# Kernel tuning notes

Hardware: AMD Instinct MI355X
Metric: run time of the kernel (lower is better)

Reference implementation:

```python
import jax, jax.numpy as jnp
import numpy as np

D_MODEL = 1024
N_HEADS = 16
HEAD_DIM = D_MODEL // N_HEADS  # 64


def setup_inputs() -> dict:
    key = jax.random.key(0)
    ks = jax.random.split(key, 6)
    scale_in = 1.0 / np.sqrt(D_MODEL)
    scale_hd = 1.0 / np.sqrt(N_HEADS * HEAD_DIM)
    inputs_q = jax.random.normal(ks[0], (4, 2048, D_MODEL), dtype=jnp.float32)
    # DenseGeneral kernels: [d_model, n_heads, head_dim] for q/k/v, [n_heads, head_dim, d_model] for out.
    Wq = jax.random.normal(ks[1], (D_MODEL, N_HEADS, HEAD_DIM), dtype=jnp.float32) * scale_in
    Wk = jax.random.normal(ks[2], (D_MODEL, N_HEADS, HEAD_DIM), dtype=jnp.float32) * scale_in
    Wv = jax.random.normal(ks[3], (D_MODEL, N_HEADS, HEAD_DIM), dtype=jnp.float32) * scale_in
    Wo = jax.random.normal(ks[4], (N_HEADS, HEAD_DIM, D_MODEL), dtype=jnp.float32) * scale_hd
    bq = jnp.zeros((N_HEADS, HEAD_DIM), dtype=jnp.float32)
    bk = jnp.zeros((N_HEADS, HEAD_DIM), dtype=jnp.float32)
    bv = jnp.zeros((N_HEADS, HEAD_DIM), dtype=jnp.float32)
    bo = jnp.zeros((D_MODEL,), dtype=jnp.float32)
    return {"inputs_q": inputs_q, "Wq": Wq, "bq": bq, "Wk": Wk, "bk": bk,
            "Wv": Wv, "bv": bv, "Wo": Wo, "bo": bo}


def reference(inputs_q, Wq, bq, Wk, bk, Wv, bv, Wo, bo):
    # Self-attention: inputs_kv = inputs_q.
    # QKV projections (DenseGeneral axis=-1 -> (heads, head_dim)).
    q = jnp.einsum('bsf,fhd->bshd', inputs_q, Wq) + bq  # [B,S,H,D]
    k = jnp.einsum('bsf,fhd->bshd', inputs_q, Wk) + bk
    v = jnp.einsum('bsf,fhd->bshd', inputs_q, Wv) + bv
    # Scaled dot-product attention (naive: full [B,H,S,S] scores, as in source).
    q = q / jnp.sqrt(jnp.asarray(HEAD_DIM, dtype=q.dtype))
    scores = jnp.einsum('bqhd,bkhd->bhqk', q, k)  # [B,H,Sq,Sk]
    attn = jax.nn.softmax(scores, axis=-1)
    x = jnp.einsum('bhqk,bkhd->bqhd', attn, v)  # [B,S,H,D]
    # Output projection over (heads, head_dim).
    out = jnp.einsum('bqhd,hdf->bqf', x, Wo) + bo  # [B,S,d_model]
    return out
```

## Files before the change

kernel.cpp:

```cpp
#include <hip/hip_runtime.h>
#include <math.h>

typedef __bf16 bf16;
typedef __attribute__((ext_vector_type(4))) __bf16 bf16x4;
typedef __attribute__((ext_vector_type(8))) __bf16 bf16x8;
typedef __attribute__((ext_vector_type(4))) float f32x4;

#define LOG2E 1.44269504088896340736f

__device__ __forceinline__ f32x4 mfma16(bf16x8 a, bf16x8 b, f32x4 c) {
  return __builtin_amdgcn_mfma_f32_16x16x32_bf16(a, b, c, 0, 0, 0);
}

__device__ __forceinline__ void load_lds16(const bf16* g, bf16* l) {
  __builtin_amdgcn_global_load_lds(
      (__attribute__((address_space(1))) void*)(g),
      (__attribute__((address_space(3))) void*)(l), 16, 0, 0);
}

__global__ __launch_bounds__(256) void prep(
    const float* __restrict__ x, const float* __restrict__ Wq,
    const float* __restrict__ Wk, const float* __restrict__ Wv,
    const float* __restrict__ Wo, bf16* __restrict__ xb,
    bf16* __restrict__ Wcat, bf16* __restrict__ WoT, float qscale) {
  __shared__ float t[32][33];
  const int z = blockIdx.z;
  const int tid = threadIdx.x;
  if (z == 4) {
    const int blk = blockIdx.y * 32 + blockIdx.x;
    const int base = blk * 8192;
#pragma unroll
    for (int u = 0; u < 4; u++) {
      int i = base + u * 2048 + tid * 8;
      float4 a = *(const float4*)&x[i];
      float4 b = *(const float4*)&x[i + 4];
      bf16x8 v;
      v[0] = (bf16)a.x; v[1] = (bf16)a.y; v[2] = (bf16)a.z; v[3] = (bf16)a.w;
      v[4] = (bf16)b.x; v[5] = (bf16)b.y; v[6] = (bf16)b.z; v[7] = (bf16)b.w;
      *(bf16x8*)&xb[i] = v;
    }
  } else {
    const float* src = (z == 0) ? Wq : (z == 1) ? Wk : (z == 2) ? Wv : Wo;
    bf16* dst = (z == 3) ? WoT : (Wcat + (size_t)z * 1024 * 1024);
    const float scale = (z == 0) ? qscale : 1.0f;
    const int tx = tid & 31, ty = tid >> 5;
    int c0 = blockIdx.x * 32, r0 = blockIdx.y * 32;
    for (int i = ty; i < 32; i += 8)
      t[i][tx] = src[(r0 + i) * 1024 + c0 + tx];
    __syncthreads();
    for (int i = ty; i < 32; i += 8)
      dst[(c0 + i) * 1024 + r0 + tx] = (bf16)(t[tx][i] * scale);
  }
}

template <int MODE>
__global__ __launch_bounds__(256, 3) void gemm_bt(
    const bf16* __restrict__ A, const bf16* __restrict__ Bt, int N, int K,
    bf16* __restrict__ Qo, bf16* __restrict__ Ko, bf16* __restrict__ Vo,
    const float* __restrict__ b0, const float* __restrict__ b1,
    const float* __restrict__ b2,
    float* __restrict__ Co, const float* __restrict__ bias) {
  __shared__ bf16 lA[2][128 * 32];
  __shared__ bf16 lB[2][128 * 32];
  const int tid = threadIdx.x;
  const int lane = tid & 63, w = tid >> 6;
  const int l16 = lane & 15, quad = lane >> 4;
  const int swz = (l16 >> 2) & 3;
  const int wm = w >> 1, wn = w & 1;
  const int id = blockIdx.x;
  const int xcd = id & 7, local = id >> 3;
  const int m0 = (xcd * 8 + (local & 7)) * 128;
  const int n0 = (local >> 3) * 128;

  const int srow = w * 16 + (lane >> 2);
  const int scol = (((lane & 3) ^ ((lane >> 4) & 3)) * 8);
  const bf16* Ag = A + (size_t)(m0 + srow) * K + scol;
  const bf16* Bg = Bt + (size_t)(n0 + srow) * K + scol;
  const int ldw = w * 16 * 32;

  load_lds16(Ag, &lA[0][ldw]);
  load_lds16(Ag + (size_t)64 * K, &lA[0][ldw + 64 * 32]);
  load_lds16(Bg, &lB[0][ldw]);
  load_lds16(Bg + (size_t)64 * K, &lB[0][ldw + 64 * 32]);

  f32x4 acc[4][4] = {};
  for (int k0 = 0; k0 < K; k0 += 32) {
    const int p = (k0 >> 5) & 1;
    __syncthreads();
    if (k0 + 32 < K) {
      load_lds16(Ag + k0 + 32, &lA[p ^ 1][ldw]);
      load_lds16(Ag + k0 + 32 + (size_t)64 * K, &lA[p ^ 1][ldw + 64 * 32]);
      load_lds16(Bg + k0 + 32, &lB[p ^ 1][ldw]);
      load_lds16(Bg + k0 + 32 + (size_t)64 * K, &lB[p ^ 1][ldw + 64 * 32]);
    }
    bf16x8 af[4], bfr[4];
#pragma unroll
    for (int i = 0; i < 4; i++)
      af[i] = *(const bf16x8*)&lA[p][(wm * 64 + i * 16 + l16) * 32 + (quad ^ swz) * 8];
#pragma unroll
    for (int i = 0; i < 4; i++)
      bfr[i] = *(const bf16x8*)&lB[p][(wn * 64 + i * 16 + l16) * 32 + (quad ^ swz) * 8];
#pragma unroll
    for (int i = 0; i < 4; i++)
#pragma unroll
      for (int j = 0; j < 4; j++)
        acc[i][j] = mfma16(bfr[j], af[i], acc[i][j]);
  }

  if (MODE == 0) {
    const int which = n0 >> 10;
    bf16* dst = (which == 0) ? Qo : (which == 1) ? Ko : Vo;
    const float* bsrc = (which == 0) ? b0 : (which == 1) ? b1 : b2;
    const float bscale = (which == 0) ? (0.125f * LOG2E) : 1.0f;
#pragma unroll
    for (int j = 0; j < 4; j++) {
      const int nn0 = (n0 & 1023) + wn * 64 + j * 16 + quad * 4;
      const int h = nn0 >> 6, d0 = nn0 & 63;
      float4 bv4 = *(const float4*)&bsrc[nn0];
#pragma unroll
      for (int i = 0; i < 4; i++) {
        const int grow = m0 + wm * 64 + i * 16 + l16;
        const int bb = grow >> 11, sq = grow & 2047;
        const size_t hb = (size_t)(bb * 16 + h) * 131072;
        if (which != 2) {
          bf16x4 pw;
          pw[0] = (bf16)(acc[i][j][0] + bv4.x * bscale);
          pw[1] = (bf16)(acc[i][j][1] + bv4.y * bscale);
          pw[2] = (bf16)(acc[i][j][2] + bv4.z * bscale);
          pw[3] = (bf16)(acc[i][j][3] + bv4.w * bscale);
          *(bf16x4*)&dst[hb + (size_t)sq * 64 + d0] = pw;
        } else {
          dst[hb + (size_t)(d0 + 0) * 2048 + sq] = (bf16)(acc[i][j][0] + bv4.x);
          dst[hb + (size_t)(d0 + 1) * 2048 + sq] = (bf16)(acc[i][j][1] + bv4.y);
          dst[hb + (size_t)(d0 + 2) * 2048 + sq] = (bf16)(acc[i][j][2] + bv4.z);
          dst[hb + (size_t)(d0 + 3) * 2048 + sq] = (bf16)(acc[i][j][3] + bv4.w);
        }
      }
    }
  } else {
#pragma unroll
    for (int j = 0; j < 4; j++) {
      const int gcol = n0 + wn * 64 + j * 16 + quad * 4;
      float4 bv4 = *(const float4*)&bias[gcol];
#pragma unroll
      for (int i = 0; i < 4; i++) {
        const int grow = m0 + wm * 64 + i * 16 + l16;
        f32x4 v = acc[i][j];
        v[0] += bv4.x; v[1] += bv4.y; v[2] += bv4.z; v[3] += bv4.w;
        *(f32x4*)&Co[(size_t)grow * N + gcol] = v;
      }
    }
  }
}

__global__ __launch_bounds__(256, 2) void attn(const bf16* __restrict__ Q,
                                               const bf16* __restrict__ Kb,
                                               const bf16* __restrict__ Vt,
                                               bf16* __restrict__ X2) {
  __shared__ bf16 lK[2][2][64][32];
  __shared__ bf16 lV[2][2][64][32];
  __shared__ bf16 lP[4][64][72];
  const int tid = threadIdx.x;
  const int lane = tid & 63, w = tid >> 6;
  const int l16 = lane & 15, quad = lane >> 4;
  const int swz = (l16 >> 2) & 3;
  const int bh = blockIdx.x & 63;
  const int q0 = (blockIdx.x >> 6) * 256;
  const int bb = bh >> 4, h = bh & 15;
  const size_t base = (size_t)bh * 2048 * 64;

  bf16x8 aq[4][2];
#pragma unroll
  for (int mi = 0; mi < 4; mi++)
#pragma unroll
    for (int kh = 0; kh < 2; kh++)
      aq[mi][kh] = *(const bf16x8*)&Q[base + (size_t)(q0 + w * 64 + mi * 16 + l16) * 64 + kh * 32 + quad * 8];

  f32x4 o_acc[4][4] = {};
  float l_r[4] = {0.f, 0.f, 0.f, 0.f};

  const int drow = lane >> 2;
  const int dcol = (((lane & 3) ^ ((lane >> 4) & 3)) * 8);
  const bf16* Kg = Kb + base + (size_t)(w * 16 + drow) * 64 + dcol;
  const bf16* Vg = Vt + base + (size_t)(w * 16 + drow) * 2048 + dcol;

  load_lds16(Kg, &lK[0][0][w * 16][0]);
  load_lds16(Kg + 32, &lK[0][1][w * 16][0]);
  load_lds16(Vg, &lV[0][0][w * 16][0]);
  load_lds16(Vg + 32, &lV[0][1][w * 16][0]);

  for (int kt = 0; kt < 32; kt++) {
    const int p = kt & 1;
    __syncthreads();
    if (kt + 1 < 32) {
      const bf16* kg = Kg + (size_t)(kt + 1) * 64 * 64;
      const bf16* vg = Vg + (kt + 1) * 64;
      load_lds16(kg, &lK[p ^ 1][0][w * 16][0]);
      load_lds16(kg + 32, &lK[p ^ 1][1][w * 16][0]);
      load_lds16(vg, &lV[p ^ 1][0][w * 16][0]);
      load_lds16(vg + 32, &lV[p ^ 1][1][w * 16][0]);
    }

#pragma unroll
    for (int g = 0; g < 2; g++) {
      f32x4 s[2][4] = {};
#pragma unroll
      for (int n2 = 0; n2 < 2; n2++) {
        const int ni = g * 2 + n2;
        bf16x8 ak0 = *(const bf16x8*)&lK[p][0][ni * 16 + l16][(quad ^ swz) * 8];
        bf16x8 ak1 = *(const bf16x8*)&lK[p][1][ni * 16 + l16][(quad ^ swz) * 8];
#pragma unroll
        for (int mi = 0; mi < 4; mi++) {
          s[n2][mi] = mfma16(ak0, aq[mi][0], s[n2][mi]);
          s[n2][mi] = mfma16(ak1, aq[mi][1], s[n2][mi]);
        }
      }
#pragma unroll
      for (int n2 = 0; n2 < 2; n2++) {
        const int ni = g * 2 + n2;
#pragma unroll
        for (int mi = 0; mi < 4; mi++) {
          bf16x4 pw;
          float lp = 0.f;
#pragma unroll
          for (int rg = 0; rg < 4; rg++) {
            float pv = __builtin_amdgcn_exp2f(s[n2][mi][rg]);
            lp += pv;
            pw[rg] = (bf16)pv;
          }
          l_r[mi] += lp;
          *(bf16x4*)&lP[w][mi * 16 + l16][ni * 16 + quad * 4] = pw;
        }
      }
    }

    bf16x8 vf0[4], vf1[4];
#pragma unroll
    for (int di = 0; di < 4; di++) {
      vf0[di] = *(const bf16x8*)&lV[p][0][di * 16 + l16][(quad ^ swz) * 8];
      vf1[di] = *(const bf16x8*)&lV[p][1][di * 16 + l16][(quad ^ swz) * 8];
    }
#pragma unroll
    for (int mi = 0; mi < 4; mi++) {
      bf16x8 ap0 = *(const bf16x8*)&lP[w][mi * 16 + l16][quad * 8];
      bf16x8 ap1 = *(const bf16x8*)&lP[w][mi * 16 + l16][32 + quad * 8];
#pragma unroll
      for (int di = 0; di < 4; di++) {
        o_acc[mi][di] = mfma16(ap0, vf0[di], o_acc[mi][di]);
        o_acc[mi][di] = mfma16(ap1, vf1[di], o_acc[mi][di]);
      }
    }
  }

#pragma unroll
  for (int mi = 0; mi < 4; mi++) {
    float l = l_r[mi];
    l += __shfl_xor(l, 16);
    l += __shfl_xor(l, 32);
    l_r[mi] = 1.f / l;
  }
#pragma unroll
  for (int mi = 0; mi < 4; mi++)
#pragma unroll
    for (int rg = 0; rg < 4; rg++) {
      float inv = __shfl(l_r[mi], quad * 4 + rg);
      int s = q0 + w * 64 + mi * 16 + quad * 4 + rg;
#pragma unroll
      for (int di = 0; di < 4; di++) {
        float v = o_acc[mi][di][rg] * inv;
        X2[((size_t)bb * 2048 + s) * 1024 + h * 64 + di * 16 + l16] = (bf16)v;
      }
    }
}

extern "C" void kernel_launch(void* const* d_in, const int* in_sizes, int n_in,
                              void* d_out, int out_size, void* d_ws, size_t ws_size,
                              hipStream_t stream) {
  const float* x  = (const float*)d_in[0];
  const float* Wq = (const float*)d_in[1];
  const float* bq = (const float*)d_in[2];
  const float* Wk = (const float*)d_in[3];
  const float* bk = (const float*)d_in[4];
  const float* Wv = (const float*)d_in[5];
  const float* bv = (const float*)d_in[6];
  const float* Wo = (const float*)d_in[7];
  const float* bo = (const float*)d_in[8];
  float* out = (float*)d_out;

  char* ws = (char*)d_ws;
  bf16* Xb   = (bf16*)(ws);
  bf16* Wcat = (bf16*)(ws + 16777216);
  bf16* WoT  = (bf16*)(ws + 23068672);
  bf16* Qb   = (bf16*)(ws + 25165824);
  bf16* Kbf  = (bf16*)(ws + 41943040);
  bf16* Vt   = (bf16*)(ws + 58720256);
  bf16* X2   = Xb;

  prep<<<dim3(32, 32, 5), 256, 0, stream>>>(
      x, Wq, Wk, Wv, Wo, Xb, Wcat, WoT, 0.125f * LOG2E);

  gemm_bt<0><<<1536, 256, 0, stream>>>(Xb, Wcat, 3072, 1024,
      Qb, Kbf, Vt, bq, bk, bv, nullptr, nullptr);

  attn<<<512, 256, 0, stream>>>(Qb, Kbf, Vt, X2);

  gemm_bt<1><<<512, 256, 0, stream>>>(X2, WoT, 1024, 1024,
      nullptr, nullptr, nullptr, nullptr, nullptr, nullptr, out, bo);
}
```

Baseline: 276.7 us.

## Add dedicated large-tile QKV GEMM kernel with 512 threads and staggered prefetch

```diff
diff --git a/kernel.cpp b/kernel.cpp
--- a/kernel.cpp
+++ b/kernel.cpp
@@ -50,6 +50,134 @@
     __syncthreads();
     for (int i = ty; i < 32; i += 8)
       dst[(c0 + i) * 1024 + r0 + tx] = (bf16)(t[tx][i] * scale);
+  }
+}
+
+__global__ __launch_bounds__(512, 2) void gemm_qkv(
+    const bf16* __restrict__ A, const bf16* __restrict__ Bt,
+    bf16* __restrict__ Qo, bf16* __restrict__ Ko, bf16* __restrict__ Vo,
+    const float* __restrict__ b0, const float* __restrict__ b1,
+    const float* __restrict__ b2) {
+  __shared__ bf16 lA[2][256 * 64];
+  __shared__ bf16 lB[2][192 * 64];
+  const int tid = threadIdx.x;
+  const int lane = tid & 63, w = tid >> 6;
+  const int l16 = lane & 15, quad = lane >> 4;
+  const int rswz = l16 & 7;
+  const int wm = w >> 2, wn = w & 3;
+  const int id = blockIdx.x;
+  const int xcd = id & 7, local = id >> 3;
+  const int m0 = (xcd * 4 + (local & 3)) * 256;
+  const int n0 = (local >> 2) * 192;
+
+  const bf16* aSrc[4];
+  const bf16* bSrc[3];
+  int aDst[4], bDst[3];
+#pragma unroll
+  for (int li = 0; li < 4; li++) {
+    int s = li * 512 + tid;
+    int r = s >> 3, c = (s & 7) ^ (r & 7);
+    aSrc[li] = A + (size_t)(m0 + r) * 1024 + c * 8;
+    aDst[li] = (li * 512 + w * 64) * 8;
+  }
+#pragma unroll
+  for (int li = 0; li < 3; li++) {
+    int s = li * 512 + tid;
+    int r = s >> 3, c = (s & 7) ^ (r & 7);
+    bSrc[li] = Bt + (size_t)(n0 + r) * 1024 + c * 8;
+    bDst[li] = (li * 512 + w * 64) * 8;
+  }
+
+#pragma unroll
+  for (int li = 0; li < 4; li++) load_lds16(aSrc[li], &lA[0][aDst[li]]);
+#pragma unroll
+  for (int li = 0; li < 3; li++) load_lds16(bSrc[li], &lB[0][bDst[li]]);
+
+  f32x4 acc[8][3] = {};
+  for (int t = 0; t < 16; t++) {
+    const int p = t & 1;
+    if (t < 15) {
+      const int k1 = (t + 1) * 64;
+#pragma unroll
+      for (int li = 0; li < 4; li++)
+        load_lds16(aSrc[li] + k1, &lA[p ^ 1][aDst[li]]);
+      asm volatile("s_waitcnt vmcnt(4)" ::: "memory");
+    } else {
+      asm volatile("s_waitcnt vmcnt(0)" ::: "memory");
+    }
+    __builtin_amdgcn_s_barrier();
+    __builtin_amdgcn_sched_barrier(0);
+
+    {
+      bf16x8 af[8], bfr[3];
+#pragma unroll
+      for (int i = 0; i < 8; i++)
+        af[i] = *(const bf16x8*)&lA[p][(wm * 128 + i * 16 + l16) * 64 + (quad ^ rswz) * 8];
+#pragma unroll
+      for (int j = 0; j < 3; j++)
+        bfr[j] = *(const bf16x8*)&lB[p][(wn * 48 + j * 16 + l16) * 64 + (quad ^ rswz) * 8];
+#pragma unroll
+      for (int i = 0; i < 8; i++)
+#pragma unroll
+        for (int j = 0; j < 3; j++)
+          acc[i][j] = mfma16(bfr[j], af[i], acc[i][j]);
+    }
+
+    if (t < 15) {
+      const int k1 = (t + 1) * 64;
+#pragma unroll
+      for (int li = 0; li < 3; li++)
+        load_lds16(bSrc[li] + k1, &lB[p ^ 1][bDst[li]]);
+    }
+
+    {
+      bf16x8 af[8], bfr[3];
+#pragma unroll
+      for (int i = 0; i < 8; i++)
+        af[i] = *(const bf16x8*)&lA[p][(wm * 128 + i * 16 + l16) * 64 + ((4 + quad) ^ rswz) * 8];
+#pragma unroll
+      for (int j = 0; j < 3; j++)
+        bfr[j] = *(const bf16x8*)&lB[p][(wn * 48 + j * 16 + l16) * 64 + ((4 + quad) ^ rswz) * 8];
+#pragma unroll
+      for (int i = 0; i < 8; i++)
+#pragma unroll
+        for (int j = 0; j < 3; j++)
+          acc[i][j] = mfma16(bfr[j], af[i], acc[i][j]);
+    }
+
+    asm volatile("" ::: "memory");
+    __builtin_amdgcn_s_barrier();
+  }
+
+#pragma unroll
+  for (int j = 0; j < 3; j++) {
+    const int nn = n0 + wn * 48 + j * 16 + quad * 4;
+    const int which = nn >> 10;
+    bf16* dst = (which == 0) ? Qo : (which == 1) ? Ko : Vo;
+    const float* bsrc = (which == 0) ? b0 : (which == 1) ? b1 : b2;
+    const float bscale = (which == 0) ? (0.125f * LOG2E) : 1.0f;
+    const int nl = nn & 1023;
+    const int h = nl >> 6, d0 = nl & 63;
+    float4 bv4 = *(const float4*)&bsrc[nl];
+#pragma unroll
+    for (int i = 0; i < 8; i++) {
+      const int grow = m0 + wm * 128 + i * 16 + l16;
+      const int bb = grow >> 11, sq = grow & 2047;
+      const size_t hb = (size_t)(bb * 16 + h) * 131072;
+      if (which != 2) {
+        bf16x4 pw;
+        pw[0] = (bf16)(acc[i][j][0] + bv4.x * bscale);
+        pw[1] = (bf16)(acc[i][j][1] + bv4.y * bscale);
+        pw[2] = (bf16)(acc[i][j][2] + bv4.z * bscale);
+        pw[3] = (bf16)(acc[i][j][3] + bv4.w * bscale);
+        *(bf16x4*)&dst[hb + (size_t)sq * 64 + d0] = pw;
+      } else {
+        dst[hb + (size_t)(d0 + 0) * 2048 + sq] = (bf16)(acc[i][j][0] + bv4.x);
+        dst[hb + (size_t)(d0 + 1) * 2048 + sq] = (bf16)(acc[i][j][1] + bv4.y);
+        dst[hb + (size_t)(d0 + 2) * 2048 + sq] = (bf16)(acc[i][j][2] + bv4.z);
+        dst[hb + (size_t)(d0 + 3) * 2048 + sq] = (bf16)(acc[i][j][3] + bv4.w);
+      }
+    }
   }
 }
 
@@ -107,37 +235,7 @@
         acc[i][j] = mfma16(bfr[j], af[i], acc[i][j]);
   }
 
-  if (MODE == 0) {
-    const int which = n0 >> 10;
-    bf16* dst = (which == 0) ? Qo : (which == 1) ? Ko : Vo;
-    const float* bsrc = (which == 0) ? b0 : (which == 1) ? b1 : b2;
-    const float bscale = (which == 0) ? (0.125f * LOG2E) : 1.0f;
-#pragma unroll
-    for (int j = 0; j < 4; j++) {
-      const int nn0 = (n0 & 1023) + wn * 64 + j * 16 + quad * 4;
-      const int h = nn0 >> 6, d0 = nn0 & 63;
-      float4 bv4 = *(const float4*)&bsrc[nn0];
-#pragma unroll
-      for (int i = 0; i < 4; i++) {
-        const int grow = m0 + wm * 64 + i * 16 + l16;
-        const int bb = grow >> 11, sq = grow & 2047;
-        const size_t hb = (size_t)(bb * 16 + h) * 131072;
-        if (which != 2) {
-          bf16x4 pw;
-          pw[0] = (bf16)(acc[i][j][0] + bv4.x * bscale);
-          pw[1] = (bf16)(acc[i][j][1] + bv4.y * bscale);
-          pw[2] = (bf16)(acc[i][j][2] + bv4.z * bscale);
-          pw[3] = (bf16)(acc[i][j][3] + bv4.w * bscale);
-          *(bf16x4*)&dst[hb + (size_t)sq * 64 + d0] = pw;
-        } else {
-          dst[hb + (size_t)(d0 + 0) * 2048 + sq] = (bf16)(acc[i][j][0] + bv4.x);
-          dst[hb + (size_t)(d0 + 1) * 2048 + sq] = (bf16)(acc[i][j][1] + bv4.y);
-          dst[hb + (size_t)(d0 + 2) * 2048 + sq] = (bf16)(acc[i][j][2] + bv4.z);
-          dst[hb + (size_t)(d0 + 3) * 2048 + sq] = (bf16)(acc[i][j][3] + bv4.w);
-        }
-      }
-    }
-  } else {
+  {
 #pragma unroll
     for (int j = 0; j < 4; j++) {
       const int gcol = n0 + wn * 64 + j * 16 + quad * 4;
@@ -299,8 +397,7 @@
   prep<<<dim3(32, 32, 5), 256, 0, stream>>>(
       x, Wq, Wk, Wv, Wo, Xb, Wcat, WoT, 0.125f * LOG2E);
 
-  gemm_bt<0><<<1536, 256, 0, stream>>>(Xb, Wcat, 3072, 1024,
-      Qb, Kbf, Vt, bq, bk, bv, nullptr, nullptr);
+  gemm_qkv<<<512, 512, 0, stream>>>(Xb, Wcat, Qb, Kbf, Vt, bq, bk, bv);
 
   attn<<<512, 256, 0, stream>>>(Qb, Kbf, Vt, X2);
 
```

Result: no change. 275.7 us (median of 2 runs) (-0.4%).

## Deepen GEMM LDS pipeline to four stages with split-phase MFMA scheduling

Applied to the files above, without the earlier changes.

```diff
diff --git a/kernel.cpp b/kernel.cpp
--- a/kernel.cpp
+++ b/kernel.cpp
@@ -54,14 +54,14 @@
 }
 
 template <int MODE>
-__global__ __launch_bounds__(256, 3) void gemm_bt(
+__global__ __launch_bounds__(256, 2) void gemm_bt(
     const bf16* __restrict__ A, const bf16* __restrict__ Bt, int N, int K,
     bf16* __restrict__ Qo, bf16* __restrict__ Ko, bf16* __restrict__ Vo,
     const float* __restrict__ b0, const float* __restrict__ b1,
     const float* __restrict__ b2,
     float* __restrict__ Co, const float* __restrict__ bias) {
-  __shared__ bf16 lA[2][128 * 32];
-  __shared__ bf16 lB[2][128 * 32];
+  __shared__ bf16 lA[4][128 * 32];
+  __shared__ bf16 lB[4][128 * 32];
   const int tid = threadIdx.x;
   const int lane = tid & 63, w = tid >> 6;
   const int l16 = lane & 15, quad = lane >> 4;
@@ -78,33 +78,67 @@
   const bf16* Bg = Bt + (size_t)(n0 + srow) * K + scol;
   const int ldw = w * 16 * 32;
 
-  load_lds16(Ag, &lA[0][ldw]);
-  load_lds16(Ag + (size_t)64 * K, &lA[0][ldw + 64 * 32]);
-  load_lds16(Bg, &lB[0][ldw]);
-  load_lds16(Bg + (size_t)64 * K, &lB[0][ldw + 64 * 32]);
+  const int nt = K >> 5;
+
+#pragma unroll
+  for (int tt = 0; tt < 3; tt++) {
+    load_lds16(Ag + tt * 32, &lA[tt][ldw]);
+    load_lds16(Ag + tt * 32 + (size_t)64 * K, &lA[tt][ldw + 64 * 32]);
+    load_lds16(Bg + tt * 32, &lB[tt][ldw]);
+    load_lds16(Bg + tt * 32 + (size_t)64 * K, &lB[tt][ldw + 64 * 32]);
+  }
 
   f32x4 acc[4][4] = {};
-  for (int k0 = 0; k0 < K; k0 += 32) {
-    const int p = (k0 >> 5) & 1;
-    __syncthreads();
-    if (k0 + 32 < K) {
-      load_lds16(Ag + k0 + 32, &lA[p ^ 1][ldw]);
-      load_lds16(Ag + k0 + 32 + (size_t)64 * K, &lA[p ^ 1][ldw + 64 * 32]);
-      load_lds16(Bg + k0 + 32, &lB[p ^ 1][ldw]);
-      load_lds16(Bg + k0 + 32 + (size_t)64 * K, &lB[p ^ 1][ldw + 64 * 32]);
-    }
+  for (int t = 0; t < nt; t++) {
+    const int p = t & 3;
+    const int ks = (t + 3) * 32;
+    if (t < nt - 2)
+      asm volatile("s_waitcnt vmcnt(8)" ::: "memory");
+    else if (t == nt - 2)
+      asm volatile("s_waitcnt vmcnt(4)" ::: "memory");
+    else
+      asm volatile("s_waitcnt vmcnt(0)" ::: "memory");
+    __builtin_amdgcn_s_barrier();
+
     bf16x8 af[4], bfr[4];
 #pragma unroll
     for (int i = 0; i < 4; i++)
       af[i] = *(const bf16x8*)&lA[p][(wm * 64 + i * 16 + l16) * 32 + (quad ^ swz) * 8];
 #pragma unroll
+    for (int j = 0; j < 2; j++)
+      bfr[j] = *(const bf16x8*)&lB[p][(wn * 64 + j * 16 + l16) * 32 + (quad ^ swz) * 8];
+    if (t + 3 < nt) {
+      load_lds16(Ag + ks, &lA[(t + 3) & 3][ldw]);
+      load_lds16(Ag + ks + (size_t)64 * K, &lA[(t + 3) & 3][ldw + 64 * 32]);
+    }
+    asm volatile("s_waitcnt lgkmcnt(0)" ::: "memory");
+    __builtin_amdgcn_sched_barrier(0);
+    __builtin_amdgcn_s_setprio(1);
+#pragma unroll
     for (int i = 0; i < 4; i++)
-      bfr[i] = *(const bf16x8*)&lB[p][(wn * 64 + i * 16 + l16) * 32 + (quad ^ swz) * 8];
+#pragma unroll
+      for (int j = 0; j < 2; j++)
+        acc[i][j] = mfma16(bfr[j], af[i], acc[i][j]);
+    __builtin_amdgcn_s_setprio(0);
+    __builtin_amdgcn_sched_barrier(0);
+
+#pragma unroll
+    for (int j = 2; j < 4; j++)
+      bfr[j] = *(const bf16x8*)&lB[p][(wn * 64 + j * 16 + l16) * 32 + (quad ^ swz) * 8];
+    if (t + 3 < nt) {
+      load_lds16(Bg + ks, &lB[(t + 3) & 3][ldw]);
+      load_lds16(Bg + ks + (size_t)64 * K, &lB[(t + 3) & 3][ldw + 64 * 32]);
+    }
+    asm volatile("s_waitcnt lgkmcnt(0)" ::: "memory");
+    __builtin_amdgcn_sched_barrier(0);
+    __builtin_amdgcn_s_setprio(1);
 #pragma unroll
     for (int i = 0; i < 4; i++)
 #pragma unroll
-      for (int j = 0; j < 4; j++)
+      for (int j = 2; j < 4; j++)
         acc[i][j] = mfma16(bfr[j], af[i], acc[i][j]);
+    __builtin_amdgcn_s_setprio(0);
+    __builtin_amdgcn_sched_barrier(0);
   }
 
   if (MODE == 0) {
```

Result: no change. 278.9 us (+0.8%).
